# Optimization experiments

Hardware: AMD Instinct MI355X
Metric: run time of the kernel (lower is better)

The kernel has to match this reference:

```python
import jax, jax.numpy as jnp
import numpy as np

B, N = 2, 6
C_IN, C_MID = 512, 512
D, C_OUT = 112, 80
OGH, OGW, DS = 256, 704, 16
FH, FW = OGH // DS, OGW // DS  # 16, 44
D_MIN, D_MAX = 2.0, 58.0
NX, NY, NZ = 128, 128, 1
VSIZE = np.array([0.8, 0.8, 8.0], dtype=np.float32)
VCOORD = np.array([-51.2 + 0.4, -51.2 + 0.4, -5.0 + 4.0], dtype=np.float32)


def make_frustum():
    # (D, FH, FW, 4) with entries (x_pix, y_pix, depth, 1)
    ones = jnp.ones((D, FH, FW), jnp.float32)
    d = jnp.linspace(D_MIN, D_MAX, D)[:, None, None] * jnp.ones((1, FH, FW))
    x = jnp.linspace(0.0, OGW - 1.0, FW)[None, None, :] * jnp.ones((D, FH, 1))
    y = jnp.linspace(0.0, OGH - 1.0, FH)[None, :, None] * jnp.ones((D, 1, FW))
    return jnp.stack([x, y, d, ones], axis=-1)


def setup_inputs() -> dict:
    key = jax.random.key(0)
    ks = jax.random.split(key, 24)
    eye = jnp.eye(4, dtype=jnp.float32)
    K = jnp.array([[1266.0, 0.0, 800.0, 0.0],
                   [0.0, 1266.0, 450.0, 0.0],
                   [0.0, 0.0, 1.0, 0.0],
                   [0.0, 0.0, 0.0, 1.0]], jnp.float32)
    inp = {
        'feat': jax.random.normal(ks[0], (B * N, C_IN, FH, FW), jnp.float32),
        'w1': 0.05 * jax.random.normal(ks[1], (C_MID, C_IN, 3, 3), jnp.float32),
        'g1': 1.0 + 0.1 * jax.random.normal(ks[2], (C_MID,), jnp.float32),
        'b1': 0.1 * jax.random.normal(ks[3], (C_MID,), jnp.float32),
        'm1': 0.1 * jax.random.normal(ks[4], (C_MID,), jnp.float32),
        'v1': 0.5 + jax.random.uniform(ks[5], (C_MID,), jnp.float32),
        'w2': 0.05 * jax.random.normal(ks[6], (C_MID, C_MID, 3, 3), jnp.float32),
        'g2': 1.0 + 0.1 * jax.random.normal(ks[7], (C_MID,), jnp.float32),
        'b2': 0.1 * jax.random.normal(ks[8], (C_MID,), jnp.float32),
        'm2': 0.1 * jax.random.normal(ks[9], (C_MID,), jnp.float32),
        'v2': 0.5 + jax.random.uniform(ks[10], (C_MID,), jnp.float32),
        'w_out': 0.05 * jax.random.normal(ks[11], (D + C_OUT, C_MID, 1, 1), jnp.float32),
        'b_out': 0.1 * jax.random.normal(ks[12], (D + C_OUT,), jnp.float32),
        'sensor2ego': eye + 0.05 * jax.random.normal(ks[13], (B, N, 4, 4), jnp.float32),
        'sensor2virtual': eye + 0.05 * jax.random.normal(ks[14], (B, N, 4, 4), jnp.float32),
        'intrin': K + 0.01 * jax.random.normal(ks[15], (B, N, 4, 4), jnp.float32),
        'ida': eye + 0.01 * jax.random.normal(ks[16], (B, N, 4, 4), jnp.float32),
        'ref_heights': 1.5 + 0.2 * jax.random.normal(ks[17], (B, N), jnp.float32),
        'bda': eye + 0.01 * jax.random.normal(ks[18], (B, 4, 4), jnp.float32),
    }
    return inp


def _conv(x, w, p):
    return jax.lax.conv_general_dilated(x, w, (1, 1), [(p, p), (p, p)],
                                         dimension_numbers=('NCHW', 'OIHW', 'NCHW'))


def _bn(x, g, b, m, v):
    s = (g / jnp.sqrt(v + 1e-5))
    return (x - m[None, :, None, None]) * s[None, :, None, None] + b[None, :, None, None]


def get_geometry(sensor2ego, sensor2virtual, intrin, ida, ref_heights, bda):
    frustum = make_frustum()[..., None]  # (D,FH,FW,4,1)
    pts = jnp.linalg.inv(ida)[:, :, None, None, None] @ frustum  # (B,N,D,FH,FW,4,1)
    ref = ref_heights[:, :, None, None, None, None]
    height = -pts[..., 2, :] + ref  # (B,N,D,FH,FW,1)
    pc = pts.at[..., 2, :].set(10.0)
    pc = jnp.concatenate([pc[..., :2, :] * pc[..., 2:3, :], pc[..., 2:, :]], axis=-2)
    cv = sensor2virtual @ jnp.linalg.inv(intrin)
    pv = cv[:, :, None, None, None] @ pc
    ratio = height[..., 0] / pv[..., 1, 0]  # (B,N,D,FH,FW)
    pts = pv * ratio[..., None, None]
    pts = pts.at[..., 3, :].set(1.0)
    ce = sensor2ego @ jnp.linalg.inv(sensor2virtual)
    pts = ce[:, :, None, None, None] @ pts
    pts = (bda[:, None, None, None, None] @ pts)[..., 0]
    return pts[..., :3]  # (B,N,D,FH,FW,3)


def reference(feat, w1, g1, b1, m1, v1, w2, g2, b2, m2, v2, w_out, b_out,
              sensor2ego, sensor2virtual, intrin, ida, ref_heights, bda):
    # DepthNet head
    h = jax.nn.relu(_bn(_conv(feat, w1, 1), g1, b1, m1, v1))
    h = jax.nn.relu(_bn(_conv(h, w2, 1), g2, b2, m2, v2))
    hf = _conv(h, w_out, 0) + b_out[None, :, None, None]  # (B*N, D+C, FH, FW)
    depth = jax.nn.softmax(hf[:, :D], axis=1).reshape(B, N, D, FH, FW)
    context = hf[:, D:].reshape(B, N, C_OUT, FH, FW)

    geom = get_geometry(sensor2ego, sensor2virtual, intrin, ida, ref_heights, bda)

    # voxel indices
    vsize = jnp.asarray(VSIZE)
    vcoord = jnp.asarray(VCOORD)
    idx = ((geom - (vcoord - vsize / 2.0)) / vsize).astype(jnp.int32)
    valid = (jnp.all(idx >= 0, axis=-1) & (idx[..., 0] < NX)
             & (idx[..., 1] < NY) & (idx[..., 2] < NZ))

    # LSS outer product: (B,N,D,FH,FW,C)
    vol = jnp.einsum('bndhw,bnchw->bndhwc', depth, context)
    YX = NY * NX
    sid = idx[..., 1] * NX + idx[..., 0] + jnp.arange(B, dtype=jnp.int32)[:, None, None, None, None] * YX
    sid = jnp.where(valid, sid, B * YX).reshape(-1)
    bev = jax.ops.segment_sum(vol.reshape(-1, C_OUT), sid, num_segments=B * YX + 1)[:B * YX]
    return bev.reshape(B, NY, NX, C_OUT).transpose(0, 3, 1, 2)  # (B,C,NY,NX)
```

## Files before the change

### kernel.cpp

```cpp
#include <hip/hip_runtime.h>
#include <stdint.h>

#define NB   2
#define NN   6
#define NIMG 12
#define CIN  512
#define CMID 512
#define DD   112
#define COUT 80
#define FHh  16
#define FWw  44
#define NPIX 704
#define NPOS 8448
#define KK   4608
#define NXg  128
#define NYg  128
#define YX   16384
#define MAT_STRIDE 56
#define PADPIX 828
#define PROW 46

typedef short short8 __attribute__((ext_vector_type(8)));
typedef float f32x4  __attribute__((ext_vector_type(4)));

#define GLD16(g, l) __builtin_amdgcn_global_load_lds((const __attribute__((address_space(1))) void*)(g), (__attribute__((address_space(3))) void*)(l), 16, 0, 0)

__device__ __forceinline__ unsigned short f2bf(float f){
  unsigned u = __float_as_uint(f);
  u += 0x7fffu + ((u >> 16) & 1u);
  return (unsigned short)(u >> 16);
}

__device__ __forceinline__ f32x4 mfma16(short8 a, short8 b, f32x4 c){
  return __builtin_amdgcn_mfma_f32_16x16x32_bf16(a, b, c, 0, 0, 0);
}

__global__ void k_f32_to_bf16(const float* __restrict__ src, unsigned short* __restrict__ dst, int n){
  for (int i = blockIdx.x*blockDim.x + threadIdx.x; i < n; i += gridDim.x*blockDim.x)
    dst[i] = f2bf(src[i]);
}

__global__ void k_wreorder(const float* __restrict__ src, unsigned short* __restrict__ dst){
  int i = blockIdx.x*blockDim.x + threadIdx.x;
  int oc = i / KK; int j = i - oc*KK;
  int r = j >> 9; int ic = j & 511;
  dst[i] = f2bf(src[(size_t)(oc*512 + ic)*9 + r]);
}

__global__ void k_bn_prep(const float* __restrict__ g, const float* __restrict__ b,
                          const float* __restrict__ m, const float* __restrict__ v,
                          float* __restrict__ scale, float* __restrict__ bias){
  int t = blockIdx.x*blockDim.x + threadIdx.x;
  if (t < CMID){
    float s = g[t] / sqrtf(v[t] + 1e-5f);
    scale[t] = s;
    bias[t]  = b[t] - m[t]*s;
  }
}

__global__ void k_featpad(const float* __restrict__ feat, unsigned short* __restrict__ dst){
  int blk = blockIdx.x;
  int img = blk >> 4, y = blk & 15;
  const float* s = feat + (size_t)img*CIN*NPIX + y*FWw;
  unsigned short* d = dst + (size_t)img*PADPIX*512 + ((y+1)*PROW + 1)*512;
  for (int j = threadIdx.x; j < FWw*512; j += 256){
    int x = j >> 9, ic = j & 511;
    d[x*512 + ic] = f2bf(s[(size_t)ic*NPIX + x]);
  }
}

__device__ void inv4(const double* A, double* out){
  double M[4][8];
  for (int i=0;i<4;i++){ for(int j=0;j<4;j++){ M[i][j]=A[i*4+j]; M[i][4+j]=(i==j)?1.0:0.0; } }
  for (int c=0;c<4;c++){
    int piv=c; double best=fabs(M[c][c]);
    for (int r=c+1;r<4;r++){ double a=fabs(M[r][c]); if(a>best){best=a;piv=r;} }
    if (piv!=c){ for(int j=0;j<8;j++){ double tt=M[c][j]; M[c][j]=M[piv][j]; M[piv][j]=tt; } }
    double inv = 1.0 / M[c][c];
    for (int j=0;j<8;j++) M[c][j]*=inv;
    for (int r=0;r<4;r++){ if(r==c) continue; double f=M[r][c];
      for (int j=0;j<8;j++) M[r][j]-=f*M[c][j]; }
  }
  for (int i=0;i<4;i++) for(int j=0;j<4;j++) out[i*4+j]=M[i][4+j];
}
__device__ void mm4(const double* A, const double* Bm, double* C){
  for (int i=0;i<4;i++) for(int j=0;j<4;j++){
    double s=0.0; for(int k=0;k<4;k++) s+=A[i*4+k]*Bm[k*4+j]; C[i*4+j]=s; }
}

__global__ void k_prep_mats(const float* __restrict__ s2e, const float* __restrict__ s2v,
                            const float* __restrict__ intr, const float* __restrict__ ida,
                            const float* __restrict__ refh, const float* __restrict__ bda,
                            double* __restrict__ mats){
  int t = threadIdx.x;
  if (t >= NIMG) return;
  int b = t / NN;
  double Mida[16], Ms2v[16], Mintr[16], Ms2e[16], Mbda[16];
  for (int i=0;i<16;i++){
    Mida[i] =(double)ida [t*16+i];
    Ms2v[i] =(double)s2v [t*16+i];
    Mintr[i]=(double)intr[t*16+i];
    Ms2e[i] =(double)s2e [t*16+i];
    Mbda[i] =(double)bda [b*16+i];
  }
  double* o = mats + (size_t)t*MAT_STRIDE;
  double tmp[16], tmp2[16];
  inv4(Mida, o);
  inv4(Mintr, tmp);  mm4(Ms2v, tmp, o+16);
  inv4(Ms2v, tmp);   mm4(Ms2e, tmp, tmp2);
  mm4(Mbda, tmp2, o+32);
  o[48] = (double)refh[t];
}

__global__ void k_geom(const double* __restrict__ mats, int* __restrict__ sid){
  int g = blockIdx.x*blockDim.x + threadIdx.x;
  int img = g / (DD*NPIX); int rem = g - img*(DD*NPIX);
  int d = rem / NPIX; int p = rem - d*NPIX;
  int h = p / FWw; int w = p - h*FWw;
  const double* M = mats + (size_t)img*MAT_STRIDE;
  float xf = (float)w * (703.0f/43.0f);
  float yf = (float)h * 17.0f;
  float df = 2.0f + (float)d * (56.0f/111.0f);
  double x = (double)xf, y = (double)yf, dep = (double)df;
  double p0 = M[0]*x + M[1]*y + M[2]*dep + M[3];
  double p1 = M[4]*x + M[5]*y + M[6]*dep + M[7];
  double p2 = M[8]*x + M[9]*y + M[10]*dep + M[11];
  double p3 = M[12]*x + M[13]*y + M[14]*dep + M[15];
  double height = M[48] - p2;
  double c0 = p0*10.0, c1 = p1*10.0, c2 = 10.0, c3 = p3;
  const double* C = M + 16;
  double q0 = C[0]*c0 + C[1]*c1 + C[2]*c2 + C[3]*c3;
  double q1 = C[4]*c0 + C[5]*c1 + C[6]*c2 + C[7]*c3;
  double q2 = C[8]*c0 + C[9]*c1 + C[10]*c2 + C[11]*c3;
  double ratio = height / q1;
  double r0 = q0*ratio, r1 = q1*ratio, r2 = q2*ratio, r3 = 1.0;
  const double* F = M + 32;
  double gx = F[0]*r0 + F[1]*r1 + F[2]*r2 + F[3]*r3;
  double gy = F[4]*r0 + F[5]*r1 + F[6]*r2 + F[7]*r3;
  double gz = F[8]*r0 + F[9]*r1 + F[10]*r2 + F[11]*r3;
  float gxf = (float)gx, gyf = (float)gy, gzf = (float)gz;
  const float vcx = (float)(-51.2 + 0.4);
  const float ox = vcx - 0.4f;
  const float oy = ox;
  const float oz = -1.0f - 4.0f;
  float tx = (gxf - ox) / 0.8f;
  float ty = (gyf - oy) / 0.8f;
  float tz = (gzf - oz) / 8.0f;
  int ix = (int)tx, iy = (int)ty, iz = (int)tz;
  bool valid = (tx==tx) && (ty==ty) && (tz==tz) &&
               (ix >= 0) && (ix < NXg) && (iy >= 0) && (iy < NYg) && (iz == 0);
  int b = img / NN;
  sid[g] = valid ? (b*YX + iy*NXg + ix) : -1;
}

template<int OUT_PADDED>
__global__ __launch_bounds__(256) void k_conv(const unsigned short* __restrict__ W,
    const unsigned short* __restrict__ src,
    const float* __restrict__ scale, const float* __restrict__ bias,
    unsigned short* __restrict__ out){
  __shared__ __align__(16) short As[128*32];
  __shared__ __align__(16) short Bs[128*32];
  int t = threadIdx.x;
  int lane = t & 63, wv = t >> 6;
  int wm = wv >> 1, wn = wv & 1;
  int q = lane >> 4, ml = lane & 15;
  int m0 = blockIdx.x * 128;
  int n0 = blockIdx.y * 128;

  int lrow = lane >> 2;
  int lcol = (lane & 3) * 8;
  const unsigned short* agp[2];
  const unsigned short* bgp[2];
  #pragma unroll
  for (int i=0;i<2;i++){
    int seg = wv*2 + i;
    agp[i] = W + (size_t)(m0 + seg*16 + lrow)*KK + lcol;
    int pos = n0 + seg*16 + lrow;
    int img = pos / NPIX; int p = pos - img*NPIX;
    int y = p / FWw; int x = p - y*FWw;
    bgp[i] = src + (size_t)img*PADPIX*512 + ((y+1)*PROW + (x+1))*512 + lcol;
  }

  f32x4 acc[4][4];
  #pragma unroll
  for (int i=0;i<4;i++)
    #pragma unroll
    for (int j=0;j<4;j++) acc[i][j] = (f32x4)0.0f;

  for (int kb = 0; kb < KK; kb += 32){
    int r = kb >> 9;
    int ic0 = kb & 511;
    int r3 = r / 3;
    int koff = (r3*PROW + (r - r3*3))*512 + ic0 - (PROW+1)*512;
    #pragma unroll
    for (int i=0;i<2;i++){
      int seg = wv*2 + i;
      GLD16(agp[i] + kb,   (char*)As + seg*1024);
      GLD16(bgp[i] + koff, (char*)Bs + seg*1024);
    }
    __syncthreads();
    short8 fa[4], fb[4];
    #pragma unroll
    for (int mi=0;mi<4;mi++) fa[mi] = *(const short8*)(As + (wm*64 + mi*16 + ml)*32 + q*8);
    #pragma unroll
    for (int ni=0;ni<4;ni++) fb[ni] = *(const short8*)(Bs + (wn*64 + ni*16 + ml)*32 + q*8);
    #pragma unroll
    for (int mi=0;mi<4;mi++)
      #pragma unroll
      for (int ni=0;ni<4;ni++)
        acc[mi][ni] = mfma16(fb[ni], fa[mi], acc[mi][ni]);
    __syncthreads();
  }

  #pragma unroll
  for (int mi=0;mi<4;mi++){
    int oc = m0 + wm*64 + mi*16 + ml;
    float s = scale[oc], bb = bias[oc];
    #pragma unroll
    for (int ni=0;ni<4;ni++){
      f32x4 v = acc[mi][ni];
      #pragma unroll
      for (int rr=0;rr<4;rr++){
        int pos = n0 + wn*64 + ni*16 + q*4 + rr;
        float val = fmaxf(v[rr]*s + bb, 0.0f);
        if (OUT_PADDED){
          int img = pos / NPIX; int p = pos - img*NPIX;
          int y = p / FWw; int x = p - y*FWw;
          out[(size_t)img*PADPIX*512 + ((y+1)*PROW + (x+1))*512 + oc] = f2bf(val);
        } else {
          out[(size_t)pos*CMID + oc] = f2bf(val);
        }
      }
    }
  }
}

__global__ __launch_bounds__(256) void k_gemm64(const unsigned short* __restrict__ A,
    const unsigned short* __restrict__ Bt, const float* __restrict__ bout,
    float* __restrict__ hf){
  const int K = 512;
  __shared__ __align__(16) short As[64][32];
  __shared__ __align__(16) short Bs[128][32];
  int t = threadIdx.x;
  int m0 = blockIdx.x*64; int n0 = blockIdx.y*128;
  int lane = t & 63; int wv = t >> 6; int q = lane >> 4, ml = lane & 15;
  f32x4 acc[8];
  #pragma unroll
  for (int i=0;i<8;i++) acc[i] = (f32x4)0.0f;
  int ar = t >> 2, ac = (t & 3) * 8;
  int br = t >> 1, bc = (t & 1) * 16;
  const unsigned short* pa = A  + (size_t)(m0 + ar)*K + ac;
  const unsigned short* pb = Bt + (size_t)(n0 + br)*K + bc;
  for (int kb = 0; kb < K; kb += 32){
    uint4 av = *(const uint4*)(pa + kb);
    uint4 b0 = *(const uint4*)(pb + kb);
    uint4 b1 = *(const uint4*)(pb + kb + 8);
    __syncthreads();
    *(uint4*)&As[ar][ac] = av;
    *(uint4*)&Bs[br][bc] = b0; *(uint4*)&Bs[br][bc+8] = b1;
    __syncthreads();
    short8 fa = *(const short8*)&As[wv*16 + ml][q*8];
    #pragma unroll
    for (int ni=0;ni<8;ni++){
      short8 fb = *(const short8*)&Bs[ni*16 + ml][q*8];
      acc[ni] = mfma16(fb, fa, acc[ni]);
    }
  }
  int oc = m0 + wv*16 + ml;
  float bb = bout[oc];
  #pragma unroll
  for (int ni=0;ni<8;ni++)
    #pragma unroll
    for (int r=0;r<4;r++){
      int pos = n0 + ni*16 + q*4 + r;
      hf[(size_t)pos*192 + oc] = acc[ni][r] + bb;
    }
}

__global__ void k_softmax(const float* __restrict__ hf, float* __restrict__ depth){
  int pos = blockIdx.x*4 + (threadIdx.x >> 6);
  int lane = threadIdx.x & 63;
  const float* row = hf + (size_t)pos*192;
  float v0 = row[lane];
  float v1 = (lane < DD-64) ? row[64 + lane] : -1e30f;
  float mx = fmaxf(v0, v1);
  #pragma unroll
  for (int m=1; m<64; m<<=1) mx = fmaxf(mx, __shfl_xor(mx, m, 64));
  float e0 = expf(v0 - mx);
  float e1 = (lane < DD-64) ? expf(v1 - mx) : 0.0f;
  float s = e0 + e1;
  #pragma unroll
  for (int m=1; m<64; m<<=1) s += __shfl_xor(s, m, 64);
  float inv = 1.0f / s;
  depth[(size_t)pos*DD + lane] = e0 * inv;
  if (lane < DD-64) depth[(size_t)pos*DD + 64 + lane] = e1 * inv;
}

__global__ void k_scatter(const float* __restrict__ depth, const float* __restrict__ hf,
                          const int* __restrict__ sidb, float* __restrict__ bev){
  int pos = blockIdx.x;
  int img = pos / NPIX; int p = pos - img*NPIX;
  __shared__ float sdep[DD];
  __shared__ float swt[DD];
  __shared__ int   ssid[DD];
  __shared__ float sctx[COUT];
  int t = threadIdx.x;
  if (t < DD){
    sdep[t] = depth[(size_t)pos*DD + t];
    ssid[t] = sidb[(size_t)(img*DD + t)*NPIX + p];
  }
  if (t < COUT) sctx[t] = hf[(size_t)pos*192 + DD + t];
  __syncthreads();
  if (t < DD){
    int s = ssid[t];
    float w = 0.0f;
    bool head = (s >= 0) && (t == 0 || ssid[t-1] != s);
    if (head){
      for (int dd = t; dd < DD && ssid[dd] == s; ++dd) w += sdep[dd];
    }
    swt[t] = head ? w : 0.0f;
  }
  __syncthreads();
  for (int j = t; j < DD*COUT; j += blockDim.x){
    int d = j / COUT, c = j - d*COUT;
    float w = swt[d];
    if (w > 0.0f) atomicAdd(&bev[(size_t)ssid[d]*COUT + c], w * sctx[c]);
  }
}

__global__ void k_transpose(const float* __restrict__ bev, float* __restrict__ out){
  int i = blockIdx.x*blockDim.x + threadIdx.x;
  int yx = i & (YX-1); int rest = i >> 14;
  int c = rest % COUT; int b = rest / COUT;
  out[i] = bev[((size_t)(b*YX + yx))*COUT + c];
}

extern "C" void kernel_launch(void* const* d_in, const int* in_sizes, int n_in,
                              void* d_out, int out_size, void* d_ws, size_t ws_size,
                              hipStream_t stream) {
  const float* feat = (const float*)d_in[0];
  const float* w1   = (const float*)d_in[1];
  const float* g1   = (const float*)d_in[2];
  const float* b1   = (const float*)d_in[3];
  const float* m1   = (const float*)d_in[4];
  const float* v1   = (const float*)d_in[5];
  const float* w2   = (const float*)d_in[6];
  const float* g2   = (const float*)d_in[7];
  const float* b2   = (const float*)d_in[8];
  const float* m2   = (const float*)d_in[9];
  const float* v2   = (const float*)d_in[10];
  const float* wout = (const float*)d_in[11];
  const float* bout = (const float*)d_in[12];
  const float* s2e  = (const float*)d_in[13];
  const float* s2v  = (const float*)d_in[14];
  const float* intr = (const float*)d_in[15];
  const float* ida  = (const float*)d_in[16];
  const float* refh = (const float*)d_in[17];
  const float* bda  = (const float*)d_in[18];

  uint8_t* base = (uint8_t*)d_ws;
  size_t off = 0;
  auto alloc = [&](size_t bytes)->void*{
    void* r = base + off;
    off = (off + bytes + 255) & ~(size_t)255;
    return r;
  };
  unsigned short* wb1 = (unsigned short*)alloc((size_t)CMID*KK*2);
  unsigned short* wb2 = (unsigned short*)alloc((size_t)CMID*KK*2);
  unsigned short* wb3 = (unsigned short*)alloc((size_t)192*CMID*2);
  float* scale1 = (float*)alloc(CMID*4);
  float* bias1  = (float*)alloc(CMID*4);
  float* scale2 = (float*)alloc(CMID*4);
  float* bias2  = (float*)alloc(CMID*4);
  double* mats  = (double*)alloc((size_t)NIMG*MAT_STRIDE*8);

  size_t padded_bytes = (size_t)NIMG*PADPIX*512*2;
  uint8_t* regionE = (uint8_t*)alloc(padded_bytes);
  uint8_t* regionF = (uint8_t*)alloc(padded_bytes);
  float* depth = (float*)alloc((size_t)NPOS*DD*4);
  int*   sid   = (int*)  alloc((size_t)NIMG*DD*NPIX*4);
  float* bev   = (float*)alloc((size_t)NB*YX*COUT*4);

  unsigned short* featpad = (unsigned short*)regionE;
  unsigned short* h2      = (unsigned short*)regionE;
  unsigned short* h1pad   = (unsigned short*)regionF;
  float*          hf      = (float*)regionF;

  k_wreorder<<<9216, 256, 0, stream>>>(w1, wb1);
  k_wreorder<<<9216, 256, 0, stream>>>(w2, wb2);
  k_f32_to_bf16<<<384, 256, 0, stream>>>(wout, wb3, 192*CMID);
  k_bn_prep<<<2, 256, 0, stream>>>(g1, b1, m1, v1, scale1, bias1);
  k_bn_prep<<<2, 256, 0, stream>>>(g2, b2, m2, v2, scale2, bias2);
  k_prep_mats<<<1, 64, 0, stream>>>(s2e, s2v, intr, ida, refh, bda, mats);
  k_geom<<<3696, 256, 0, stream>>>(mats, sid);

  hipMemsetAsync(featpad, 0, padded_bytes, stream);
  hipMemsetAsync(h1pad,   0, padded_bytes, stream);
  k_featpad<<<192, 256, 0, stream>>>(feat, featpad);

  k_conv<1><<<dim3(4, 66), 256, 0, stream>>>(wb1, featpad, scale1, bias1, h1pad);
  k_conv<0><<<dim3(4, 66), 256, 0, stream>>>(wb2, h1pad, scale2, bias2, h2);
  k_gemm64<<<dim3(3, 66), 256, 0, stream>>>(wb3, h2, bout, hf);

  k_softmax<<<2112, 256, 0, stream>>>(hf, depth);

  hipMemsetAsync(bev, 0, (size_t)NB*YX*COUT*4, stream);
  k_scatter<<<NPOS, 256, 0, stream>>>(depth, hf, sid, bev);

  k_transpose<<<10240, 256, 0, stream>>>(bev, (float*)d_out);
}
```

Before: 457.8 us.

## Pipeline conv loads with 4-stage async buffers in single-wave blocks; compact scatter list

```diff
diff --git a/kernel.cpp b/kernel.cpp
--- a/kernel.cpp
+++ b/kernel.cpp
@@ -154,31 +154,27 @@
 }
 
 template<int OUT_PADDED>
-__global__ __launch_bounds__(256) void k_conv(const unsigned short* __restrict__ W,
+__global__ __launch_bounds__(64) void k_conv_p(const unsigned short* __restrict__ W,
     const unsigned short* __restrict__ src,
     const float* __restrict__ scale, const float* __restrict__ bias,
     unsigned short* __restrict__ out){
-  __shared__ __align__(16) short As[128*32];
-  __shared__ __align__(16) short Bs[128*32];
-  int t = threadIdx.x;
-  int lane = t & 63, wv = t >> 6;
-  int wm = wv >> 1, wn = wv & 1;
+  __shared__ __align__(16) short As[4*64*32];
+  __shared__ __align__(16) short Bs[4*64*32];
+  int lane = threadIdx.x;
   int q = lane >> 4, ml = lane & 15;
-  int m0 = blockIdx.x * 128;
-  int n0 = blockIdx.y * 128;
+  int m0 = blockIdx.x * 64;
+  int n0 = blockIdx.y * 64;
 
   int lrow = lane >> 2;
-  int lcol = (lane & 3) * 8;
-  const unsigned short* agp[2];
-  const unsigned short* bgp[2];
-  #pragma unroll
-  for (int i=0;i<2;i++){
-    int seg = wv*2 + i;
-    agp[i] = W + (size_t)(m0 + seg*16 + lrow)*KK + lcol;
-    int pos = n0 + seg*16 + lrow;
+  int lch  = (lane & 3) * 8;
+  const unsigned short* aptr = W + (size_t)(m0 + lrow)*KK + lch;
+  const unsigned short* bptr[4];
+  #pragma unroll
+  for (int i=0;i<4;i++){
+    int pos = n0 + i*16 + lrow;
     int img = pos / NPIX; int p = pos - img*NPIX;
     int y = p / FWw; int x = p - y*FWw;
-    bgp[i] = src + (size_t)img*PADPIX*512 + ((y+1)*PROW + (x+1))*512 + lcol;
+    bptr[i] = src + (size_t)img*PADPIX*512 + ((y+1)*PROW + (x+1))*512 + lch;
   }
 
   f32x4 acc[4][4];
@@ -187,41 +183,49 @@
     #pragma unroll
     for (int j=0;j<4;j++) acc[i][j] = (f32x4)0.0f;
 
-  for (int kb = 0; kb < KK; kb += 32){
-    int r = kb >> 9;
-    int ic0 = kb & 511;
-    int r3 = r / 3;
+  auto stage = [&](int s, int d){
+    int kb = s*32;
+    int r = kb >> 9, ic0 = kb & 511;
+    int r3 = r/3;
     int koff = (r3*PROW + (r - r3*3))*512 + ic0 - (PROW+1)*512;
     #pragma unroll
-    for (int i=0;i<2;i++){
-      int seg = wv*2 + i;
-      GLD16(agp[i] + kb,   (char*)As + seg*1024);
-      GLD16(bgp[i] + koff, (char*)Bs + seg*1024);
+    for (int i=0;i<4;i++){
+      GLD16(aptr + (size_t)i*16*KK + kb, (char*)As + d*4096 + i*1024);
+      GLD16(bptr[i] + koff,              (char*)Bs + d*4096 + i*1024);
     }
-    __syncthreads();
+  };
+
+  const int NSTEP = KK/32;
+  stage(0,0); stage(1,1); stage(2,2); stage(3,3);
+
+  for (int k = 0; k < NSTEP; ++k){
+    int d = k & 3;
+    asm volatile("s_waitcnt vmcnt(24)" ::: "memory");
+    const short* Ab = As + d*2048;
+    const short* Bb = Bs + d*2048;
     short8 fa[4], fb[4];
     #pragma unroll
-    for (int mi=0;mi<4;mi++) fa[mi] = *(const short8*)(As + (wm*64 + mi*16 + ml)*32 + q*8);
-    #pragma unroll
-    for (int ni=0;ni<4;ni++) fb[ni] = *(const short8*)(Bs + (wn*64 + ni*16 + ml)*32 + q*8);
+    for (int mi=0;mi<4;mi++) fa[mi] = *(const short8*)(Ab + (mi*16 + ml)*32 + q*8);
+    #pragma unroll
+    for (int ni=0;ni<4;ni++) fb[ni] = *(const short8*)(Bb + (ni*16 + ml)*32 + q*8);
     #pragma unroll
     for (int mi=0;mi<4;mi++)
       #pragma unroll
       for (int ni=0;ni<4;ni++)
         acc[mi][ni] = mfma16(fb[ni], fa[mi], acc[mi][ni]);
-    __syncthreads();
+    if (k + 4 < NSTEP) stage(k + 4, d);
   }
 
   #pragma unroll
   for (int mi=0;mi<4;mi++){
-    int oc = m0 + wm*64 + mi*16 + ml;
+    int oc = m0 + mi*16 + ml;
     float s = scale[oc], bb = bias[oc];
     #pragma unroll
     for (int ni=0;ni<4;ni++){
       f32x4 v = acc[mi][ni];
       #pragma unroll
       for (int rr=0;rr<4;rr++){
-        int pos = n0 + wn*64 + ni*16 + q*4 + rr;
+        int pos = n0 + ni*16 + q*4 + rr;
         float val = fmaxf(v[rr]*s + bb, 0.0f);
         if (OUT_PADDED){
           int img = pos / NPIX; int p = pos - img*NPIX;
@@ -301,10 +305,13 @@
   int pos = blockIdx.x;
   int img = pos / NPIX; int p = pos - img*NPIX;
   __shared__ float sdep[DD];
-  __shared__ float swt[DD];
   __shared__ int   ssid[DD];
   __shared__ float sctx[COUT];
+  __shared__ float cwt[DD];
+  __shared__ int   cvox[DD];
+  __shared__ int   scnt;
   int t = threadIdx.x;
+  if (t == 0) scnt = 0;
   if (t < DD){
     sdep[t] = depth[(size_t)pos*DD + t];
     ssid[t] = sidb[(size_t)(img*DD + t)*NPIX + p];
@@ -313,18 +320,19 @@
   __syncthreads();
   if (t < DD){
     int s = ssid[t];
-    float w = 0.0f;
     bool head = (s >= 0) && (t == 0 || ssid[t-1] != s);
     if (head){
+      float w = 0.0f;
       for (int dd = t; dd < DD && ssid[dd] == s; ++dd) w += sdep[dd];
+      int i = atomicAdd(&scnt, 1);
+      cvox[i] = s; cwt[i] = w;
     }
-    swt[t] = head ? w : 0.0f;
   }
   __syncthreads();
-  for (int j = t; j < DD*COUT; j += blockDim.x){
-    int d = j / COUT, c = j - d*COUT;
-    float w = swt[d];
-    if (w > 0.0f) atomicAdd(&bev[(size_t)ssid[d]*COUT + c], w * sctx[c]);
+  int H = scnt;
+  for (int j = t; j < H*COUT; j += 128){
+    int h = j / COUT, c = j - h*COUT;
+    atomicAdd(&bev[(size_t)cvox[h]*COUT + c], cwt[h]*sctx[c]);
   }
 }
 
@@ -398,14 +406,14 @@
   hipMemsetAsync(h1pad,   0, padded_bytes, stream);
   k_featpad<<<192, 256, 0, stream>>>(feat, featpad);
 
-  k_conv<1><<<dim3(4, 66), 256, 0, stream>>>(wb1, featpad, scale1, bias1, h1pad);
-  k_conv<0><<<dim3(4, 66), 256, 0, stream>>>(wb2, h1pad, scale2, bias2, h2);
+  k_conv_p<1><<<dim3(8, 132), 64, 0, stream>>>(wb1, featpad, scale1, bias1, h1pad);
+  k_conv_p<0><<<dim3(8, 132), 64, 0, stream>>>(wb2, h1pad, scale2, bias2, h2);
   k_gemm64<<<dim3(3, 66), 256, 0, stream>>>(wb3, h2, bout, hf);
 
   k_softmax<<<2112, 256, 0, stream>>>(hf, depth);
 
   hipMemsetAsync(bev, 0, (size_t)NB*YX*COUT*4, stream);
-  k_scatter<<<NPOS, 256, 0, stream>>>(depth, hf, sid, bev);
+  k_scatter<<<NPOS, 128, 0, stream>>>(depth, hf, sid, bev);
 
   k_transpose<<<10240, 256, 0, stream>>>(bev, (float*)d_out);
 }
```

After: 583.6 us. 27.5% more time.

## Split-K the 3x3 convolutions and compact scatter heads in shared memory

Applied to the files above, without the earlier changes.

```diff
diff --git a/kernel.cpp b/kernel.cpp
--- a/kernel.cpp
+++ b/kernel.cpp
@@ -19,6 +19,8 @@
 #define MAT_STRIDE 56
 #define PADPIX 828
 #define PROW 46
+#define KSPLIT 4
+#define KCHUNK (KK/KSPLIT)
 
 typedef short short8 __attribute__((ext_vector_type(8)));
 typedef float f32x4  __attribute__((ext_vector_type(4)));
@@ -153,11 +155,8 @@
   sid[g] = valid ? (b*YX + iy*NXg + ix) : -1;
 }
 
-template<int OUT_PADDED>
-__global__ __launch_bounds__(256) void k_conv(const unsigned short* __restrict__ W,
-    const unsigned short* __restrict__ src,
-    const float* __restrict__ scale, const float* __restrict__ bias,
-    unsigned short* __restrict__ out){
+__global__ __launch_bounds__(256, 4) void k_conv_sk(const unsigned short* __restrict__ W,
+    const unsigned short* __restrict__ src, float* __restrict__ part){
   __shared__ __align__(16) short As[128*32];
   __shared__ __align__(16) short Bs[128*32];
   int t = threadIdx.x;
@@ -166,6 +165,7 @@
   int q = lane >> 4, ml = lane & 15;
   int m0 = blockIdx.x * 128;
   int n0 = blockIdx.y * 128;
+  int k0 = blockIdx.z * KCHUNK;
 
   int lrow = lane >> 2;
   int lcol = (lane & 3) * 8;
@@ -187,7 +187,7 @@
     #pragma unroll
     for (int j=0;j<4;j++) acc[i][j] = (f32x4)0.0f;
 
-  for (int kb = 0; kb < KK; kb += 32){
+  for (int kb = k0; kb < k0 + KCHUNK; kb += 32){
     int r = kb >> 9;
     int ic0 = kb & 511;
     int r3 = r / 3;
@@ -212,26 +212,38 @@
     __syncthreads();
   }
 
+  float* op = part + (size_t)blockIdx.z*NPOS*CMID;
   #pragma unroll
   for (int mi=0;mi<4;mi++){
     int oc = m0 + wm*64 + mi*16 + ml;
-    float s = scale[oc], bb = bias[oc];
     #pragma unroll
     for (int ni=0;ni<4;ni++){
       f32x4 v = acc[mi][ni];
       #pragma unroll
       for (int rr=0;rr<4;rr++){
         int pos = n0 + wn*64 + ni*16 + q*4 + rr;
-        float val = fmaxf(v[rr]*s + bb, 0.0f);
-        if (OUT_PADDED){
-          int img = pos / NPIX; int p = pos - img*NPIX;
-          int y = p / FWw; int x = p - y*FWw;
-          out[(size_t)img*PADPIX*512 + ((y+1)*PROW + (x+1))*512 + oc] = f2bf(val);
-        } else {
-          out[(size_t)pos*CMID + oc] = f2bf(val);
-        }
+        op[(size_t)pos*CMID + oc] = v[rr];
       }
     }
+  }
+}
+
+template<int OUT_PADDED>
+__global__ void k_reduce(const float* __restrict__ part,
+                         const float* __restrict__ scale, const float* __restrict__ bias,
+                         unsigned short* __restrict__ out){
+  int i = blockIdx.x*blockDim.x + threadIdx.x;
+  int pos = i >> 9, oc = i & 511;
+  const size_t S = (size_t)NPOS*CMID;
+  float sum = part[i] + part[i + S] + part[i + 2*S] + part[i + 3*S];
+  float val = fmaxf(sum*scale[oc] + bias[oc], 0.0f);
+  unsigned short bv = f2bf(val);
+  if (OUT_PADDED){
+    int img = pos / NPIX; int p = pos - img*NPIX;
+    int y = p / FWw; int x = p - y*FWw;
+    out[(size_t)img*PADPIX*512 + ((y+1)*PROW + (x+1))*512 + oc] = bv;
+  } else {
+    out[i] = bv;
   }
 }
 
@@ -301,10 +313,13 @@
   int pos = blockIdx.x;
   int img = pos / NPIX; int p = pos - img*NPIX;
   __shared__ float sdep[DD];
-  __shared__ float swt[DD];
   __shared__ int   ssid[DD];
   __shared__ float sctx[COUT];
+  __shared__ float cwt[DD];
+  __shared__ int   cvox[DD];
+  __shared__ int   scnt;
   int t = threadIdx.x;
+  if (t == 0) scnt = 0;
   if (t < DD){
     sdep[t] = depth[(size_t)pos*DD + t];
     ssid[t] = sidb[(size_t)(img*DD + t)*NPIX + p];
@@ -313,18 +328,19 @@
   __syncthreads();
   if (t < DD){
     int s = ssid[t];
-    float w = 0.0f;
     bool head = (s >= 0) && (t == 0 || ssid[t-1] != s);
     if (head){
+      float w = 0.0f;
       for (int dd = t; dd < DD && ssid[dd] == s; ++dd) w += sdep[dd];
+      int i = atomicAdd(&scnt, 1);
+      cvox[i] = s; cwt[i] = w;
     }
-    swt[t] = head ? w : 0.0f;
   }
   __syncthreads();
-  for (int j = t; j < DD*COUT; j += blockDim.x){
-    int d = j / COUT, c = j - d*COUT;
-    float w = swt[d];
-    if (w > 0.0f) atomicAdd(&bev[(size_t)ssid[d]*COUT + c], w * sctx[c]);
+  int H = scnt;
+  for (int j = t; j < H*COUT; j += 128){
+    int h = j / COUT, c = j - h*COUT;
+    atomicAdd(&bev[(size_t)cvox[h]*COUT + c], cwt[h]*sctx[c]);
   }
 }
 
@@ -380,6 +396,7 @@
   float* depth = (float*)alloc((size_t)NPOS*DD*4);
   int*   sid   = (int*)  alloc((size_t)NIMG*DD*NPIX*4);
   float* bev   = (float*)alloc((size_t)NB*YX*COUT*4);
+  float* part  = (float*)alloc((size_t)KSPLIT*NPOS*CMID*4);
 
   unsigned short* featpad = (unsigned short*)regionE;
   unsigned short* h2      = (unsigned short*)regionE;
@@ -398,14 +415,16 @@
   hipMemsetAsync(h1pad,   0, padded_bytes, stream);
   k_featpad<<<192, 256, 0, stream>>>(feat, featpad);
 
-  k_conv<1><<<dim3(4, 66), 256, 0, stream>>>(wb1, featpad, scale1, bias1, h1pad);
-  k_conv<0><<<dim3(4, 66), 256, 0, stream>>>(wb2, h1pad, scale2, bias2, h2);
+  k_conv_sk<<<dim3(4, 66, KSPLIT), 256, 0, stream>>>(wb1, featpad, part);
+  k_reduce<1><<<16896, 256, 0, stream>>>(part, scale1, bias1, h1pad);
+  k_conv_sk<<<dim3(4, 66, KSPLIT), 256, 0, stream>>>(wb2, h1pad, part);
+  k_reduce<0><<<16896, 256, 0, stream>>>(part, scale2, bias2, h2);
   k_gemm64<<<dim3(3, 66), 256, 0, stream>>>(wb3, h2, bout, hf);
 
   k_softmax<<<2112, 256, 0, stream>>>(hf, depth);
 
   hipMemsetAsync(bev, 0, (size_t)NB*YX*COUT*4, stream);
-  k_scatter<<<NPOS, 256, 0, stream>>>(depth, hf, sid, bev);
+  k_scatter<<<NPOS, 128, 0, stream>>>(depth, hf, sid, bev);
 
   k_transpose<<<10240, 256, 0, stream>>>(bev, (float*)d_out);
 }
```

New measurement: 424.0 us. 1.08x faster.
